# Performance work log

Measured on AMD Instinct MI355X. Metric: run time of the kernel, lower is better.

## Reference

```python
import jax, jax.numpy as jnp
import numpy as np
from jax import lax

E, L, S, F = 4, 8, 512, 32
SAMPLE_SIZE = 512
BATCH_LEN = 64
TRAIN_ENVS = [0, 1, 2]


def setup_inputs() -> dict:
    key = jax.random.key(0)
    k1, k2 = jax.random.split(key)
    data_len = jax.random.randint(k2, (E, L), S // 2, S + 1).astype(jnp.int32)
    matrix = jax.random.normal(k1, (E, L, S, F), dtype=jnp.float32)
    # zero-pad samples beyond each (env,label) length, as shape_to_matrix does
    mask = (jnp.arange(S)[None, None, :, None] < data_len[:, :, None, None])
    matrix = matrix * mask.astype(jnp.float32)
    params = jnp.eye(F, dtype=jnp.float32)
    return {"matrix": matrix, "params": params, "data_len": data_len}


def _pair_indices():
    train_idx, test_idx = [], []
    for i in range(E):
        for j in range(E):
            idx = i * E + j
            if i < j:
                test_idx.append(idx)
                if i in TRAIN_ENVS and j in TRAIN_ENVS:
                    train_idx.append(idx)
    return np.array(train_idx), np.array(test_idx)


def reference(matrix, params, data_len):
    # normalize by mean per-(env,label,feature) std (torch.std is unbiased -> ddof=1)
    std = jnp.std(matrix, axis=2, ddof=1).mean()
    m = matrix / std
    bw = 1.06 * (S ** (-1.0 / 5.0)) * jnp.std(m, axis=2, ddof=1).mean()
    lenf = data_len.astype(jnp.float32)                     # [E,L]
    proj = jnp.einsum('elsf,fg->elsg', m, params)           # [E,L,S,F]

    left = lax.stop_gradient(proj.min())
    right = lax.stop_gradient(proj.max())
    delta = (right - left) / SAMPLE_SIZE
    grid = jnp.linspace(left, right, SAMPLE_SIZE)           # [G]
    divisor = jnp.sqrt(2.0 * jnp.pi) * bw

    n_chunks = SAMPLE_SIZE // BATCH_LEN
    grid_chunks = grid.reshape(n_chunks, BATCH_LEN)
    inv2bw2 = 0.5 / (bw * bw)
    pad_count = (float(S) - lenf)[:, :, None, None]         # [E,L,1,1]
    lend = lenf[:, :, None, None]

    def step(carry, pts):
        # Gaussian KDE kernel: offset^(d^2) == exp(-0.5*d^2/bw^2)
        d2 = (proj[..., None] - pts) ** 2                   # [E,L,S,F,C]
        ksum = jnp.exp(-inv2bw2 * d2).sum(axis=2)           # [E,L,F,C]
        corr = pad_count * jnp.exp(-inv2bw2 * pts ** 2)     # zero-padding correction
        red = (ksum - corr) / lend                          # [E,L,F,C]
        diff = jnp.abs(red[:, None] - red[None, :]).sum(-1) # [E,E,L,F]
        return carry + diff, None

    store, _ = lax.scan(step, jnp.zeros((E, E, L, F), dtype=proj.dtype), grid_chunks)
    store_dis = (store / divisor).reshape(E * E, L, F)

    train_idx, test_idx = _pair_indices()
    test_results = (store_dis[test_idx] * delta / 2.0).max(axis=0)    # [L,F]
    train_results = (store_dis[train_idx] * delta / 2.0).max(axis=0)  # [L,F]
    train_dis = train_results.max(axis=0).mean()
    test_dis = test_results.max(axis=0).mean()
    return train_results, test_results, train_dis, test_dis
```

## Files before the change

### kernel.cpp

```cpp
#include <hip/hip_runtime.h>
#include <float.h>


#if __has_builtin(__builtin_amdgcn_exp2f)
__device__ __forceinline__ float fast_exp2(float x) { return __builtin_amdgcn_exp2f(x); }
#else
__device__ __forceinline__ float fast_exp2(float x) { return exp2f(x); }
#endif

#define PT_OFF    0
#define SX_OFF    524288
#define SXX_OFF   532480
#define MIN_OFF   540672
#define MAX_OFF   540928
#define CONST_OFF 541184
#define PAIR_OFF  541200


__global__ __launch_bounds__(256) void stage_prep(const float* __restrict__ matrix,
                                                  const float* __restrict__ params,
                                                  float* __restrict__ PT,
                                                  float* __restrict__ sxg,
                                                  float* __restrict__ sxxg,
                                                  float* __restrict__ minp,
                                                  float* __restrict__ maxp) {
    __shared__ float M[64][33];
    __shared__ float Pm[32][32];
    __shared__ float sxr[8][32], sxxr[8][32];
    __shared__ float rmin[4], rmax[4];
    const int bid = blockIdx.x;
    const int s0 = (bid & 7) << 6;
    const int el = bid >> 3;
    const int t = threadIdx.x;
    for (int k = t; k < 1024; k += 256) Pm[k >> 5][k & 31] = params[k];
    const float* mb = matrix + (size_t)(el * 512 + s0) * 32;
    for (int k = t; k < 2048; k += 256) M[k >> 5][k & 31] = mb[k];
    __syncthreads();
    {
        const int f = t & 31, r = t >> 5;
        float sx = 0.f, sxx = 0.f;
        #pragma unroll
        for (int k = 0; k < 8; ++k) {
            float v = M[r * 8 + k][f];
            sx += v; sxx += v * v;
        }
        sxr[r][f] = sx; sxxr[r][f] = sxx;
    }
    const int s = t & 63;
    const int g0 = t >> 6;
    float lmin = FLT_MAX, lmax = -FLT_MAX;
    #pragma unroll
    for (int pass = 0; pass < 8; ++pass) {
        const int g = (pass << 2) + g0;
        float acc = 0.f;
        #pragma unroll
        for (int fp = 0; fp < 32; ++fp) acc += M[s][fp] * Pm[fp][g];
        lmin = fminf(lmin, acc);
        lmax = fmaxf(lmax, acc);
        PT[(size_t)(el * 32 + g) * 512 + s0 + s] = acc;
    }
    #pragma unroll
    for (int off = 32; off >= 1; off >>= 1) {
        lmin = fminf(lmin, __shfl_xor(lmin, off, 64));
        lmax = fmaxf(lmax, __shfl_xor(lmax, off, 64));
    }
    if ((t & 63) == 0) { rmin[t >> 6] = lmin; rmax[t >> 6] = lmax; }
    __syncthreads();
    if (t < 32) {
        float a = 0.f, b = 0.f;
        #pragma unroll
        for (int r = 0; r < 8; ++r) { a += sxr[r][t]; b += sxxr[r][t]; }
        sxg[bid * 32 + t] = a;
        sxxg[bid * 32 + t] = b;
    }
    if (t == 0) {
        minp[bid] = fminf(fminf(rmin[0], rmin[1]), fminf(rmin[2], rmin[3]));
        maxp[bid] = fmaxf(fmaxf(rmax[0], rmax[1]), fmaxf(rmax[2], rmax[3]));
    }
}

__global__ __launch_bounds__(512) void stage_consts(const float* __restrict__ sxg,
                                                    const float* __restrict__ sxxg,
                                                    const float* __restrict__ minp,
                                                    const float* __restrict__ maxp,
                                                    float* __restrict__ consts) {
    const int t = threadIdx.x;
    __shared__ float wsum[8], wmin[8], wmax[8];
    float stdloc = 0.f;
    #pragma unroll
    for (int tr = t; tr < 1024; tr += 512) {
        const int el = tr >> 5, f = tr & 31;
        const int base = el * 256 + f;
        float sx = 0.f, sxx = 0.f;
        #pragma unroll
        for (int tile = 0; tile < 8; ++tile) { sx += sxg[base + tile * 32]; sxx += sxxg[base + tile * 32]; }
        float mean = sx * (1.0f / 512.0f);
        float var = (sxx - sx * mean) * (1.0f / 511.0f);
        stdloc += sqrtf(fmaxf(var, 0.f));
    }
    float mn = (t < 256) ? minp[t] : FLT_MAX;
    float mx = (t < 256) ? maxp[t] : -FLT_MAX;
    #pragma unroll
    for (int off = 32; off >= 1; off >>= 1) {
        stdloc += __shfl_xor(stdloc, off, 64);
        mn = fminf(mn, __shfl_xor(mn, off, 64));
        mx = fmaxf(mx, __shfl_xor(mx, off, 64));
    }
    if ((t & 63) == 0) { wsum[t >> 6] = stdloc; wmin[t >> 6] = mn; wmax[t >> 6] = mx; }
    __syncthreads();
    if (t == 0) {
        float s = 0.f, lo = FLT_MAX, hi = -FLT_MAX;
        #pragma unroll
        for (int w = 0; w < 8; ++w) { s += wsum[w]; lo = fminf(lo, wmin[w]); hi = fmaxf(hi, wmax[w]); }
        const float stdv = s * (1.0f / 1024.0f);
        const float left  = lo / stdv;
        const float right = hi / stdv;
        const float bw = 1.06f * 0.28717458874925877f;
        const float delta = (right - left) * (1.0f / 512.0f);
        const float gstep = (right - left) * (1.0f / 511.0f);
        const float divisor = 2.5066282746310002f * bw;
        const float inv2bw2 = 0.5f / (bw * bw);
        consts[0] = stdv;
        consts[1] = 1.0f / stdv;
        consts[2] = left;
        consts[3] = right;
        consts[4] = delta;
        consts[5] = delta * 0.5f / divisor;
        consts[6] = -(inv2bw2 * 1.4426950408889634f);
        consts[7] = gstep;
    }
}

__global__ __launch_bounds__(512) void stage_kde(const float* __restrict__ PT,
                                                 const int* __restrict__ data_len,
                                                 const float* __restrict__ consts,
                                                 float* __restrict__ pair_out) {
    const int bid = blockIdx.x;
    const int lf = bid >> 2, chunk = bid & 3;
    const int l = lf >> 5, f = lf & 31;
    const int t = threadIdx.x;
    const int e = t >> 7, gl = t & 127;
    __shared__ __align__(16) float xs[4][512];
    __shared__ __align__(16) float ys[4][512];
    __shared__ float sred[4][128];
    __shared__ float wred2[6][2];
    const float invstd = consts[1];
    const float left   = consts[2];
    const float negc   = consts[6];
    const float gstep  = consts[7];
    #pragma unroll
    for (int e2 = 0; e2 < 4; ++e2) {
        float v = PT[((size_t)(((e2 << 3) + l) * 32 + f) << 9) + t] * invstd;
        xs[e2][t] = v;
        ys[e2][t] = negc * v * v;
    }
    __syncthreads();
    const int g = (chunk << 7) + gl;
    const float p = fmaf((float)g, gstep, left);
    const float B = -2.0f * negc * p;
    const float C = negc * p * p;
    const int len = data_len[(e << 3) + l];
    const float* __restrict__ x = xs[e];
    const float* __restrict__ y = ys[e];
    float a0 = 0.f, a1 = 0.f, a2 = 0.f, a3 = 0.f;
    int s = 0;
    for (; s + 8 <= len; s += 8) {
        float4 xv0 = *reinterpret_cast<const float4*>(&x[s]);
        float4 xv1 = *reinterpret_cast<const float4*>(&x[s + 4]);
        float4 yv0 = *reinterpret_cast<const float4*>(&y[s]);
        float4 yv1 = *reinterpret_cast<const float4*>(&y[s + 4]);
        a0 += fast_exp2(fmaf(B, xv0.x, yv0.x) + C);
        a1 += fast_exp2(fmaf(B, xv0.y, yv0.y) + C);
        a2 += fast_exp2(fmaf(B, xv0.z, yv0.z) + C);
        a3 += fast_exp2(fmaf(B, xv0.w, yv0.w) + C);
        a0 += fast_exp2(fmaf(B, xv1.x, yv1.x) + C);
        a1 += fast_exp2(fmaf(B, xv1.y, yv1.y) + C);
        a2 += fast_exp2(fmaf(B, xv1.z, yv1.z) + C);
        a3 += fast_exp2(fmaf(B, xv1.w, yv1.w) + C);
    }
    for (; s < len; ++s)
        a0 += fast_exp2(fmaf(B, x[s], y[s]) + C);
    sred[e][gl] = ((a0 + a1) + (a2 + a3)) / (float)len;
    __syncthreads();
    if (t < 128) {
        const float r0 = sred[0][t], r1 = sred[1][t], r2 = sred[2][t], r3 = sred[3][t];
        float pr[6];
        pr[0] = fabsf(r0 - r1);
        pr[1] = fabsf(r0 - r2);
        pr[2] = fabsf(r0 - r3);
        pr[3] = fabsf(r1 - r2);
        pr[4] = fabsf(r1 - r3);
        pr[5] = fabsf(r2 - r3);
        #pragma unroll
        for (int pi = 0; pi < 6; ++pi) {
            float v = pr[pi];
            #pragma unroll
            for (int off = 32; off >= 1; off >>= 1) v += __shfl_xor(v, off, 64);
            if ((t & 63) == 0) wred2[pi][t >> 6] = v;
        }
    }
    __syncthreads();
    if (t < 6) pair_out[t * 1024 + bid] = wred2[t][0] + wred2[t][1];
}

__global__ __launch_bounds__(256) void stage_final(const float* __restrict__ pair_out,
                                                   const float* __restrict__ consts,
                                                   float* __restrict__ out) {
    const int t = threadIdx.x;
    const float scale = consts[5];
    float v[6];
    #pragma unroll
    for (int pi = 0; pi < 6; ++pi) {
        float s = 0.f;
        #pragma unroll
        for (int c = 0; c < 4; ++c) s += pair_out[pi * 1024 + t * 4 + c];
        v[pi] = s * scale;
    }
    float testv = v[0];
    #pragma unroll
    for (int pi = 1; pi < 6; ++pi) testv = fmaxf(testv, v[pi]);
    const float trainv = fmaxf(fmaxf(v[0], v[1]), v[3]);
    out[t] = trainv;
    out[256 + t] = testv;
    __shared__ float str[256], ste[256];
    str[t] = trainv; ste[t] = testv;
    __syncthreads();
    if (t < 32) {
        float mt = str[t], me = ste[t];
        for (int lrow = 1; lrow < 8; ++lrow) {
            mt = fmaxf(mt, str[lrow * 32 + t]);
            me = fmaxf(me, ste[lrow * 32 + t]);
        }
        str[t] = mt; ste[t] = me;
    }
    __syncthreads();
    if (t == 0) {
        float smt = 0.f, sme = 0.f;
        for (int k = 0; k < 32; ++k) { smt += str[k]; sme += ste[k]; }
        out[512] = smt * (1.0f / 32.0f);
        out[513] = sme * (1.0f / 32.0f);
    }
}

extern "C" void kernel_launch(void* const* d_in, const int* in_sizes, int n_in,
                              void* d_out, int out_size, void* d_ws, size_t ws_size,
                              hipStream_t stream) {
    (void)in_sizes; (void)n_in; (void)out_size; (void)ws_size;
    const float* matrix = (const float*)d_in[0];
    const float* params = (const float*)d_in[1];
    const int*   dlen   = (const int*)d_in[2];
    float* out = (float*)d_out;
    float* ws  = (float*)d_ws;
    float* PT      = ws + PT_OFF;
    float* sxg     = ws + SX_OFF;
    float* sxxg    = ws + SXX_OFF;
    float* minp    = ws + MIN_OFF;
    float* maxp    = ws + MAX_OFF;
    float* consts  = ws + CONST_OFF;
    float* pairsum = ws + PAIR_OFF;

    hipLaunchKernelGGL(stage_prep,   dim3(256),  dim3(256), 0, stream,
                       matrix, params, PT, sxg, sxxg, minp, maxp);
    hipLaunchKernelGGL(stage_consts, dim3(1),    dim3(512), 0, stream,
                       sxg, sxxg, minp, maxp, consts);
    hipLaunchKernelGGL(stage_kde,    dim3(1024), dim3(512), 0, stream,
                       PT, dlen, consts, pairsum);
    hipLaunchKernelGGL(stage_final,  dim3(1),    dim3(256), 0, stream,
                       pairsum, consts, out);
}
```

Measured before the change: 102.2 us.

## Fuse consts, KDE and final reduction into one kernel with last-block finalize

Merges the constants kernel, the KDE kernel and the final reduction into one kernel, cutting four launches to two. Each block now recomputes the global std/min/max constants redundantly, handles one (l,f) pair with 1024 threads over all 512 grid points (two per thread), and the last block, found through an atomic counter, computes the final means. The exponent is rewritten as exp2(-(x-p)^2) with pre-scaled inputs, which drops the y array and one FMA per term. The cost is redundant constant computation in every block, only 256 blocks, and an atomic-counter handshake for the finalize step.

```diff
diff --git a/kernel.cpp b/kernel.cpp
--- a/kernel.cpp
+++ b/kernel.cpp
@@ -13,9 +13,7 @@
 #define SXX_OFF   532480
 #define MIN_OFF   540672
 #define MAX_OFF   540928
-#define CONST_OFF 541184
-#define PAIR_OFF  541200
-
+#define CNT_OFF   541184
 
 __global__ __launch_bounds__(256) void stage_prep(const float* __restrict__ matrix,
                                                   const float* __restrict__ params,
@@ -23,7 +21,8 @@
                                                   float* __restrict__ sxg,
                                                   float* __restrict__ sxxg,
                                                   float* __restrict__ minp,
-                                                  float* __restrict__ maxp) {
+                                                  float* __restrict__ maxp,
+                                                  int* __restrict__ counter) {
     __shared__ float M[64][33];
     __shared__ float Pm[32][32];
     __shared__ float sxr[8][32], sxxr[8][32];
@@ -32,6 +31,7 @@
     const int s0 = (bid & 7) << 6;
     const int el = bid >> 3;
     const int t = threadIdx.x;
+    if (bid == 0 && t == 0) *counter = 0;
     for (int k = t; k < 1024; k += 256) Pm[k >> 5][k & 31] = params[k];
     const float* mb = matrix + (size_t)(el * 512 + s0) * 32;
     for (int k = t; k < 2048; k += 256) M[k >> 5][k & 31] = mb[k];
@@ -79,111 +79,104 @@
     }
 }
 
-__global__ __launch_bounds__(512) void stage_consts(const float* __restrict__ sxg,
-                                                    const float* __restrict__ sxxg,
-                                                    const float* __restrict__ minp,
-                                                    const float* __restrict__ maxp,
-                                                    float* __restrict__ consts) {
+__global__ __launch_bounds__(1024, 4) void stage_kde2(const float* __restrict__ PT,
+                                                      const float* __restrict__ sxg,
+                                                      const float* __restrict__ sxxg,
+                                                      const float* __restrict__ minp,
+                                                      const float* __restrict__ maxp,
+                                                      const int* __restrict__ dlen,
+                                                      int* __restrict__ counter,
+                                                      float* __restrict__ out) {
+    __shared__ __align__(16) float xs[4][512];
+    __shared__ float red[4][512];
+    __shared__ float wsum[16], wmn[16], wmx[16];
+    __shared__ float wred[8][6];
+    __shared__ float csh[6];
+    __shared__ int lastf;
     const int t = threadIdx.x;
-    __shared__ float wsum[8], wmin[8], wmax[8];
-    float stdloc = 0.f;
+    const int lf = blockIdx.x;
+    const int l = lf >> 5, f = lf & 31;
+
+    {
+        const int el = t >> 5, fc = t & 31;
+        const int base = el * 256 + fc;
+        float Sx = 0.f, Sxx = 0.f;
+        #pragma unroll
+        for (int tile = 0; tile < 8; ++tile) { Sx += sxg[base + tile * 32]; Sxx += sxxg[base + tile * 32]; }
+        const float mean = Sx * (1.0f / 512.0f);
+        const float var = (Sxx - Sx * mean) * (1.0f / 511.0f);
+        float sf = sqrtf(fmaxf(var, 0.f));
+        float mn = (t < 256) ? minp[t] : FLT_MAX;
+        float mx = (t < 256) ? maxp[t] : -FLT_MAX;
+        #pragma unroll
+        for (int off = 32; off >= 1; off >>= 1) {
+            sf += __shfl_xor(sf, off, 64);
+            mn = fminf(mn, __shfl_xor(mn, off, 64));
+            mx = fmaxf(mx, __shfl_xor(mx, off, 64));
+        }
+        if ((t & 63) == 0) { wsum[t >> 6] = sf; wmn[t >> 6] = mn; wmx[t >> 6] = mx; }
+        __syncthreads();
+        if (t == 0) {
+            float s = 0.f, lo = FLT_MAX, hi = -FLT_MAX;
+            #pragma unroll
+            for (int w = 0; w < 16; ++w) {
+                s += wsum[w]; lo = fminf(lo, wmn[w]); hi = fmaxf(hi, wmx[w]);
+            }
+            const float stdv = s * (1.0f / 1024.0f);
+            const float left  = lo / stdv;
+            const float right = hi / stdv;
+            const float bw = 1.06f * 0.28717458874925877f;
+            const float delta = (right - left) * (1.0f / 512.0f);
+            const float gstep = (right - left) * (1.0f / 511.0f);
+            const float divisor = 2.5066282746310002f * bw;
+            const float cpos = (0.5f / (bw * bw)) * 1.4426950408889634f;
+            const float kf = sqrtf(cpos);
+            csh[0] = left;
+            csh[1] = gstep;
+            csh[2] = kf;
+            csh[3] = (1.0f / stdv) * kf;
+            csh[4] = delta * 0.5f / divisor;
+        }
+    }
+    __syncthreads();
+    const float left = csh[0], gstep = csh[1], kf = csh[2], xscale = csh[3];
+
     #pragma unroll
-    for (int tr = t; tr < 1024; tr += 512) {
-        const int el = tr >> 5, f = tr & 31;
-        const int base = el * 256 + f;
-        float sx = 0.f, sxx = 0.f;
-        #pragma unroll
-        for (int tile = 0; tile < 8; ++tile) { sx += sxg[base + tile * 32]; sxx += sxxg[base + tile * 32]; }
-        float mean = sx * (1.0f / 512.0f);
-        float var = (sxx - sx * mean) * (1.0f / 511.0f);
-        stdloc += sqrtf(fmaxf(var, 0.f));
-    }
-    float mn = (t < 256) ? minp[t] : FLT_MAX;
-    float mx = (t < 256) ? maxp[t] : -FLT_MAX;
-    #pragma unroll
-    for (int off = 32; off >= 1; off >>= 1) {
-        stdloc += __shfl_xor(stdloc, off, 64);
-        mn = fminf(mn, __shfl_xor(mn, off, 64));
-        mx = fmaxf(mx, __shfl_xor(mx, off, 64));
-    }
-    if ((t & 63) == 0) { wsum[t >> 6] = stdloc; wmin[t >> 6] = mn; wmax[t >> 6] = mx; }
-    __syncthreads();
-    if (t == 0) {
-        float s = 0.f, lo = FLT_MAX, hi = -FLT_MAX;
-        #pragma unroll
-        for (int w = 0; w < 8; ++w) { s += wsum[w]; lo = fminf(lo, wmin[w]); hi = fmaxf(hi, wmax[w]); }
-        const float stdv = s * (1.0f / 1024.0f);
-        const float left  = lo / stdv;
-        const float right = hi / stdv;
-        const float bw = 1.06f * 0.28717458874925877f;
-        const float delta = (right - left) * (1.0f / 512.0f);
-        const float gstep = (right - left) * (1.0f / 511.0f);
-        const float divisor = 2.5066282746310002f * bw;
-        const float inv2bw2 = 0.5f / (bw * bw);
-        consts[0] = stdv;
-        consts[1] = 1.0f / stdv;
-        consts[2] = left;
-        consts[3] = right;
-        consts[4] = delta;
-        consts[5] = delta * 0.5f / divisor;
-        consts[6] = -(inv2bw2 * 1.4426950408889634f);
-        consts[7] = gstep;
-    }
-}
-
-__global__ __launch_bounds__(512) void stage_kde(const float* __restrict__ PT,
-                                                 const int* __restrict__ data_len,
-                                                 const float* __restrict__ consts,
-                                                 float* __restrict__ pair_out) {
-    const int bid = blockIdx.x;
-    const int lf = bid >> 2, chunk = bid & 3;
-    const int l = lf >> 5, f = lf & 31;
-    const int t = threadIdx.x;
-    const int e = t >> 7, gl = t & 127;
-    __shared__ __align__(16) float xs[4][512];
-    __shared__ __align__(16) float ys[4][512];
-    __shared__ float sred[4][128];
-    __shared__ float wred2[6][2];
-    const float invstd = consts[1];
-    const float left   = consts[2];
-    const float negc   = consts[6];
-    const float gstep  = consts[7];
-    #pragma unroll
-    for (int e2 = 0; e2 < 4; ++e2) {
-        float v = PT[((size_t)(((e2 << 3) + l) * 32 + f) << 9) + t] * invstd;
-        xs[e2][t] = v;
-        ys[e2][t] = negc * v * v;
-    }
-    __syncthreads();
-    const int g = (chunk << 7) + gl;
-    const float p = fmaf((float)g, gstep, left);
-    const float B = -2.0f * negc * p;
-    const float C = negc * p * p;
-    const int len = data_len[(e << 3) + l];
+    for (int k = t; k < 2048; k += 1024) {
+        const int e2 = k >> 9, s2 = k & 511;
+        xs[e2][s2] = PT[((size_t)(((e2 << 3) + l) * 32 + f) << 9) + s2] * xscale;
+    }
+    __syncthreads();
+
+    const int e = t >> 8, gl = t & 255;
+    const int len = dlen[(e << 3) + l];
+    const float pa = fmaf((float)gl, gstep, left) * kf;
+    const float pb = fmaf((float)(gl + 256), gstep, left) * kf;
     const float* __restrict__ x = xs[e];
-    const float* __restrict__ y = ys[e];
-    float a0 = 0.f, a1 = 0.f, a2 = 0.f, a3 = 0.f;
+    float2 A0 = {0.f, 0.f}, A1 = {0.f, 0.f}, A2 = {0.f, 0.f}, A3 = {0.f, 0.f};
     int s = 0;
-    for (; s + 8 <= len; s += 8) {
-        float4 xv0 = *reinterpret_cast<const float4*>(&x[s]);
-        float4 xv1 = *reinterpret_cast<const float4*>(&x[s + 4]);
-        float4 yv0 = *reinterpret_cast<const float4*>(&y[s]);
-        float4 yv1 = *reinterpret_cast<const float4*>(&y[s + 4]);
-        a0 += fast_exp2(fmaf(B, xv0.x, yv0.x) + C);
-        a1 += fast_exp2(fmaf(B, xv0.y, yv0.y) + C);
-        a2 += fast_exp2(fmaf(B, xv0.z, yv0.z) + C);
-        a3 += fast_exp2(fmaf(B, xv0.w, yv0.w) + C);
-        a0 += fast_exp2(fmaf(B, xv1.x, yv1.x) + C);
-        a1 += fast_exp2(fmaf(B, xv1.y, yv1.y) + C);
-        a2 += fast_exp2(fmaf(B, xv1.z, yv1.z) + C);
-        a3 += fast_exp2(fmaf(B, xv1.w, yv1.w) + C);
-    }
-    for (; s < len; ++s)
-        a0 += fast_exp2(fmaf(B, x[s], y[s]) + C);
-    sred[e][gl] = ((a0 + a1) + (a2 + a3)) / (float)len;
-    __syncthreads();
-    if (t < 128) {
-        const float r0 = sred[0][t], r1 = sred[1][t], r2 = sred[2][t], r3 = sred[3][t];
+    for (; s + 4 <= len; s += 4) {
+        const float4 v = *reinterpret_cast<const float4*>(&x[s]);
+        const float d0a = v.x - pa, d0b = v.x - pb;
+        const float d1a = v.y - pa, d1b = v.y - pb;
+        const float d2a = v.z - pa, d2b = v.z - pb;
+        const float d3a = v.w - pa, d3b = v.w - pb;
+        A0.x += fast_exp2(-(d0a * d0a)); A0.y += fast_exp2(-(d0b * d0b));
+        A1.x += fast_exp2(-(d1a * d1a)); A1.y += fast_exp2(-(d1b * d1b));
+        A2.x += fast_exp2(-(d2a * d2a)); A2.y += fast_exp2(-(d2b * d2b));
+        A3.x += fast_exp2(-(d3a * d3a)); A3.y += fast_exp2(-(d3b * d3b));
+    }
+    for (; s < len; ++s) {
+        const float da = x[s] - pa, db = x[s] - pb;
+        A0.x += fast_exp2(-(da * da)); A0.y += fast_exp2(-(db * db));
+    }
+    const float inv_len = 1.0f / (float)len;
+    red[e][gl]       = ((A0.x + A1.x) + (A2.x + A3.x)) * inv_len;
+    red[e][gl + 256] = ((A0.y + A1.y) + (A2.y + A3.y)) * inv_len;
+    __syncthreads();
+
+    if (t < 512) {
+        const float r0 = red[0][t], r1 = red[1][t], r2 = red[2][t], r3 = red[3][t];
         float pr[6];
         pr[0] = fabsf(r0 - r1);
         pr[1] = fabsf(r0 - r2);
@@ -196,49 +189,46 @@
             float v = pr[pi];
             #pragma unroll
             for (int off = 32; off >= 1; off >>= 1) v += __shfl_xor(v, off, 64);
-            if ((t & 63) == 0) wred2[pi][t >> 6] = v;
-        }
-    }
-    __syncthreads();
-    if (t < 6) pair_out[t * 1024 + bid] = wred2[t][0] + wred2[t][1];
-}
-
-__global__ __launch_bounds__(256) void stage_final(const float* __restrict__ pair_out,
-                                                   const float* __restrict__ consts,
-                                                   float* __restrict__ out) {
-    const int t = threadIdx.x;
-    const float scale = consts[5];
-    float v[6];
-    #pragma unroll
-    for (int pi = 0; pi < 6; ++pi) {
-        float s = 0.f;
-        #pragma unroll
-        for (int c = 0; c < 4; ++c) s += pair_out[pi * 1024 + t * 4 + c];
-        v[pi] = s * scale;
-    }
-    float testv = v[0];
-    #pragma unroll
-    for (int pi = 1; pi < 6; ++pi) testv = fmaxf(testv, v[pi]);
-    const float trainv = fmaxf(fmaxf(v[0], v[1]), v[3]);
-    out[t] = trainv;
-    out[256 + t] = testv;
-    __shared__ float str[256], ste[256];
-    str[t] = trainv; ste[t] = testv;
-    __syncthreads();
-    if (t < 32) {
-        float mt = str[t], me = ste[t];
-        for (int lrow = 1; lrow < 8; ++lrow) {
-            mt = fmaxf(mt, str[lrow * 32 + t]);
-            me = fmaxf(me, ste[lrow * 32 + t]);
-        }
-        str[t] = mt; ste[t] = me;
+            if ((t & 63) == 0) wred[t >> 6][pi] = v;
+        }
     }
     __syncthreads();
     if (t == 0) {
-        float smt = 0.f, sme = 0.f;
-        for (int k = 0; k < 32; ++k) { smt += str[k]; sme += ste[k]; }
-        out[512] = smt * (1.0f / 32.0f);
-        out[513] = sme * (1.0f / 32.0f);
+        const float scale = csh[4];
+        float v[6];
+        #pragma unroll
+        for (int pi = 0; pi < 6; ++pi) {
+            float sm = 0.f;
+            #pragma unroll
+            for (int w = 0; w < 8; ++w) sm += wred[w][pi];
+            v[pi] = sm * scale;
+        }
+        float testv = v[0];
+        #pragma unroll
+        for (int pi = 1; pi < 6; ++pi) testv = fmaxf(testv, v[pi]);
+        const float trainv = fmaxf(fmaxf(v[0], v[1]), v[3]);
+        out[lf] = trainv;
+        out[256 + lf] = testv;
+        __threadfence();
+        const int old = __hip_atomic_fetch_add(counter, 1, __ATOMIC_ACQ_REL,
+                                               __HIP_MEMORY_SCOPE_AGENT);
+        lastf = (old == 255);
+    }
+    __syncthreads();
+
+    if (lastf && t < 64) {
+        const int ff = t & 31;
+        const int base = (t >= 32) ? 256 : 0;
+        float m = -FLT_MAX;
+        #pragma unroll
+        for (int ll = 0; ll < 8; ++ll) {
+            const float val = __hip_atomic_load(&out[base + ll * 32 + ff],
+                                                __ATOMIC_RELAXED, __HIP_MEMORY_SCOPE_AGENT);
+            m = fmaxf(m, val);
+        }
+        #pragma unroll
+        for (int off = 16; off >= 1; off >>= 1) m += __shfl_xor(m, off, 32);
+        if (ff == 0) out[512 + (base ? 1 : 0)] = m * (1.0f / 32.0f);
     }
 }
 
@@ -251,20 +241,15 @@
     const int*   dlen   = (const int*)d_in[2];
     float* out = (float*)d_out;
     float* ws  = (float*)d_ws;
-    float* PT      = ws + PT_OFF;
-    float* sxg     = ws + SX_OFF;
-    float* sxxg    = ws + SXX_OFF;
-    float* minp    = ws + MIN_OFF;
-    float* maxp    = ws + MAX_OFF;
-    float* consts  = ws + CONST_OFF;
-    float* pairsum = ws + PAIR_OFF;
-
-    hipLaunchKernelGGL(stage_prep,   dim3(256),  dim3(256), 0, stream,
-                       matrix, params, PT, sxg, sxxg, minp, maxp);
-    hipLaunchKernelGGL(stage_consts, dim3(1),    dim3(512), 0, stream,
-                       sxg, sxxg, minp, maxp, consts);
-    hipLaunchKernelGGL(stage_kde,    dim3(1024), dim3(512), 0, stream,
-                       PT, dlen, consts, pairsum);
-    hipLaunchKernelGGL(stage_final,  dim3(1),    dim3(256), 0, stream,
-                       pairsum, consts, out);
+    float* PT   = ws + PT_OFF;
+    float* sxg  = ws + SX_OFF;
+    float* sxxg = ws + SXX_OFF;
+    float* minp = ws + MIN_OFF;
+    float* maxp = ws + MAX_OFF;
+    int*   cnt  = (int*)(ws + CNT_OFF);
+
+    hipLaunchKernelGGL(stage_prep, dim3(256), dim3(256), 0, stream,
+                       matrix, params, PT, sxg, sxxg, minp, maxp, cnt);
+    hipLaunchKernelGGL(stage_kde2, dim3(256), dim3(1024), 0, stream,
+                       PT, sxg, sxxg, minp, maxp, dlen, cnt, out);
 }
```

Result: no change. 102.3 us (+0.1%).
